# Kernel tuning notes

Measured on AMD Instinct MI355X. Metric: run time of the kernel, lower is better.

## Reference

```python
import jax, jax.numpy as jnp
import numpy as np

NUM_CITIES = 50000
EMB = 50   # embedding dim (hardcoded in module)
HID = 64   # LSTM hidden size (hardcoded in module)
BATCH = 1024
SEQ = 512


def setup_inputs() -> dict:
    key = jax.random.key(0)
    ks = jax.random.split(key, 8)
    s = 0.1
    return {
        "x": jax.random.randint(ks[0], (BATCH, SEQ), 0, NUM_CITIES),
        "emb": jax.random.normal(ks[1], (NUM_CITIES, EMB), jnp.float32) * s,
        # PyTorch LSTM weight layout: [4*H, in] with gate order i, f, g, o
        "W_ih": jax.random.normal(ks[2], (4 * HID, EMB), jnp.float32) * s,
        "W_hh": jax.random.normal(ks[3], (4 * HID, HID), jnp.float32) * s,
        "b_ih": jax.random.normal(ks[4], (4 * HID,), jnp.float32) * s,
        "b_hh": jax.random.normal(ks[5], (4 * HID,), jnp.float32) * s,
        "W_fc": jax.random.normal(ks[6], (NUM_CITIES, HID), jnp.float32) * s,
        "b_fc": jax.random.normal(ks[7], (NUM_CITIES,), jnp.float32) * s,
    }


def _lstm_last_hidden(e, W_ih, W_hh, b):
    """Run single-layer LSTM (zero init state), return final hidden h_T. e: [B,S,EMB]."""
    # Precompute all input-side gate projections in one big GEMM: [B,S,4H]
    gx = jnp.einsum('bsi,gi->bsg', e, W_ih) + b
    B = e.shape[0]
    H = W_hh.shape[1]
    W_hh_T = W_hh.T  # [H, 4H]
    h0 = jnp.zeros((B, H), e.dtype)
    c0 = jnp.zeros((B, H), e.dtype)

    def step(carry, gx_t):
        h, c = carry
        g = gx_t + h @ W_hh_T  # [B, 4H]
        i, f, gg, o = jnp.split(g, 4, axis=-1)
        i = jax.nn.sigmoid(i)
        f = jax.nn.sigmoid(f)
        gg = jnp.tanh(gg)
        o = jax.nn.sigmoid(o)
        c = f * c + i * gg
        h = o * jnp.tanh(c)
        return (h, c), None

    (h, c), _ = jax.lax.scan(step, (h0, c0), jnp.swapaxes(gx, 0, 1))
    return h  # [B, H]


def reference(x, emb, W_ih, W_hh, b_ih, b_hh, W_fc, b_fc):
    e = emb[x]                                   # [B, S, EMB] embedding lookup
    h = _lstm_last_hidden(e, W_ih, W_hh, b_ih + b_hh)  # [B, H]
    logits = h @ W_fc.T + b_fc                   # [B, NUM_CITIES]
    return jax.nn.softmax(logits, axis=1)
```

## Files before the change

### kernel.cpp

```cpp
#include <hip/hip_runtime.h>

#define BATCH 1024
#define SEQN  512
#define EMBD  50
#define HID   64
#define NC    50000
#define RPBK  2
#define HSTR  72
#define ESTR  72
#define CHUNK 16
#define NBLKX ((NC + 255) / 256)

typedef _Float16 half8 __attribute__((ext_vector_type(8)));
typedef float    f32x4 __attribute__((ext_vector_type(4)));

__device__ __forceinline__ void barrier_lds_only() {
    asm volatile("s_waitcnt lgkmcnt(0)\n\ts_barrier" ::: "memory");
}

__global__ __launch_bounds__(256, 2)
void lstm_rec(const int* __restrict__ x, const float* __restrict__ emb,
              const float* __restrict__ W_ih, const float* __restrict__ W_hh,
              const float* __restrict__ b_ih, const float* __restrict__ b_hh,
              _Float16* __restrict__ hFh)
{
    __shared__ __align__(16) _Float16 HS[2][16][HSTR];
    __shared__ __align__(16) _Float16 ER[2][CHUNK][RPBK][ESTR];
    __shared__ int xbuf[RPBK * SEQN];

    const int t    = threadIdx.x;
    const int w    = t >> 6;
    const int lane = t & 63;
    const int q    = lane >> 4;
    const int cc   = lane & 15;
    const int r0   = blockIdx.x * RPBK;
    const int u    = 16 * w + cc;

    half8 Bh[2][4], Bi[2][4];
    float bias[4];
#pragma unroll
    for (int nt = 0; nt < 4; ++nt) {
        const int g = 64 * nt + u;
        bias[nt] = b_ih[g] + b_hh[g];
#pragma unroll
        for (int kt = 0; kt < 2; ++kt)
#pragma unroll
            for (int j = 0; j < 8; ++j) {
                const int k = 32 * kt + 8 * q + j;
                Bh[kt][nt][j] = (_Float16)W_hh[g * HID + k];
                Bi[kt][nt][j] = (k < EMBD) ? (_Float16)W_ih[g * EMBD + k] : (_Float16)0.0f;
            }
    }

    for (int i = t; i < RPBK * SEQN; i += 256)
        xbuf[i] = x[(size_t)(r0 + (i >> 9)) * SEQN + (i & (SEQN - 1))];
    {
        _Float16* hz = &HS[0][0][0];
        for (int i = t; i < 2 * 16 * HSTR; i += 256) hz[i] = (_Float16)0.0f;
        _Float16* ez = &ER[0][0][0][0];
        for (int i = t; i < 2 * CHUNK * RPBK * ESTR; i += 256) ez[i] = (_Float16)0.0f;
    }
    __syncthreads();

    float ge[7];
#define GATHER(CH) do {                                                         \
        const int sb_ = (CH) * CHUNK;                                           \
        _Pragma("unroll")                                                       \
        for (int i = 0; i < 7; ++i) {                                           \
            const int idx = t + 256 * i;                                        \
            if (idx < CHUNK * RPBK * EMBD) {                                    \
                const int st_ = idx / (RPBK * EMBD);                            \
                const int rm_ = idx % (RPBK * EMBD);                            \
                const int rw_ = rm_ / EMBD;                                     \
                const int dm_ = rm_ % EMBD;                                     \
                int ss_ = sb_ + st_; if (ss_ > SEQN - 1) ss_ = SEQN - 1;        \
                ge[i] = emb[(size_t)xbuf[rw_ * SEQN + ss_] * EMBD + dm_];       \
            }                                                                   \
        }                                                                       \
    } while (0)
#define RINGW(CH) do {                                                          \
        const int hf_ = (CH) & 1;                                               \
        _Pragma("unroll")                                                       \
        for (int i = 0; i < 7; ++i) {                                           \
            const int idx = t + 256 * i;                                        \
            if (idx < CHUNK * RPBK * EMBD) {                                    \
                const int st_ = idx / (RPBK * EMBD);                            \
                const int rm_ = idx % (RPBK * EMBD);                            \
                const int rw_ = rm_ / EMBD;                                     \
                const int dm_ = rm_ % EMBD;                                     \
                ER[hf_][st_][rw_][dm_] = (_Float16)ge[i];                       \
            }                                                                   \
        }                                                                       \
    } while (0)

    GATHER(0);
    RINGW(0);
    GATHER(1);
    barrier_lds_only();

    float cst0 = 0.0f, cst1 = 0.0f;

    for (int s = 0; s < SEQN; ++s) {
        const int pb = s & 1;
        const int hf = (s >> 4) & 1;
        const int st = s & 15;
        const int er = cc & 1;

        const half8 Ae0 = *(const half8*)&ER[hf][st][er][8 * q];
        const half8 Ae1 = *(const half8*)&ER[hf][st][er][32 + 8 * q];
        const half8 Ah0 = *(const half8*)&HS[pb][cc][8 * q];
        const half8 Ah1 = *(const half8*)&HS[pb][cc][32 + 8 * q];

        f32x4 acc[4];
#pragma unroll
        for (int nt = 0; nt < 4; ++nt) {
            f32x4 z = (f32x4){0.f, 0.f, 0.f, 0.f};
            z = __builtin_amdgcn_mfma_f32_16x16x32_f16(Ae0, Bi[0][nt], z, 0, 0, 0);
            z = __builtin_amdgcn_mfma_f32_16x16x32_f16(Ae1, Bi[1][nt], z, 0, 0, 0);
            z = __builtin_amdgcn_mfma_f32_16x16x32_f16(Ah0, Bh[0][nt], z, 0, 0, 0);
            acc[nt] = __builtin_amdgcn_mfma_f32_16x16x32_f16(Ah1, Bh[1][nt], z, 0, 0, 0);
        }

        if (q == 0) {
            float p0[4], p1[4];
#pragma unroll
            for (int nt = 0; nt < 4; ++nt) {
                p0[nt] = acc[nt][0] + bias[nt];
                p1[nt] = acc[nt][1] + bias[nt];
            }
            const float i0 = __builtin_amdgcn_rcpf(1.0f + __expf(-p0[0]));
            const float f0 = __builtin_amdgcn_rcpf(1.0f + __expf(-p0[1]));
            const float g0 = 1.0f - 2.0f * __builtin_amdgcn_rcpf(__expf(2.0f * p0[2]) + 1.0f);
            const float o0 = __builtin_amdgcn_rcpf(1.0f + __expf(-p0[3]));
            const float i1 = __builtin_amdgcn_rcpf(1.0f + __expf(-p1[0]));
            const float f1 = __builtin_amdgcn_rcpf(1.0f + __expf(-p1[1]));
            const float g1 = 1.0f - 2.0f * __builtin_amdgcn_rcpf(__expf(2.0f * p1[2]) + 1.0f);
            const float o1 = __builtin_amdgcn_rcpf(1.0f + __expf(-p1[3]));
            cst0 = fmaf(f0, cst0, i0 * g0);
            cst1 = fmaf(f1, cst1, i1 * g1);
            const float h0 = o0 * (1.0f - 2.0f * __builtin_amdgcn_rcpf(__expf(2.0f * cst0) + 1.0f));
            const float h1 = o1 * (1.0f - 2.0f * __builtin_amdgcn_rcpf(__expf(2.0f * cst1) + 1.0f));
            HS[pb ^ 1][0][u] = (_Float16)h0;
            HS[pb ^ 1][1][u] = (_Float16)h1;
            if (s == SEQN - 1) {
                hFh[(size_t)r0 * HID + u]       = (_Float16)h0;
                hFh[(size_t)(r0 + 1) * HID + u] = (_Float16)h1;
            }
        }

        if (st == CHUNK - 1) {
            const int ch = s >> 4;
            RINGW(ch + 1);
            GATHER(ch + 2);
        }

        barrier_lds_only();
    }
#undef GATHER
#undef RINGW
}

__global__ __launch_bounds__(256, 2)
void fc_exp(const _Float16* __restrict__ hFh, const float* __restrict__ W_fc,
            const float* __restrict__ b_fc, float* __restrict__ Sp,
            float* __restrict__ out)
{
    __shared__ float sred[4][64];
    const int t    = threadIdx.x;
    const int w    = t >> 6;
    const int lane = t & 63;
    const int q    = lane >> 4;
    const int cc   = lane & 15;
    const int n0   = blockIdx.x * 256;

    half8 Bf[4][2];
    float bias[4];
#pragma unroll
    for (int nt = 0; nt < 4; ++nt) {
        int n = n0 + 64 * w + 16 * nt + cc;
        const int nl = (n < NC) ? n : NC - 1;
        bias[nt] = b_fc[nl];
#pragma unroll
        for (int kt = 0; kt < 2; ++kt) {
            const float* p = W_fc + (size_t)nl * HID + 32 * kt + 8 * q;
#pragma unroll
            for (int j = 0; j < 8; ++j) Bf[nt][kt][j] = (_Float16)p[j];
        }
    }

    const int rg0 = blockIdx.y * 8;
    for (int rg = rg0; rg < rg0 + 8; ++rg) {
        const int row0 = rg * 64;

        half8 Af[4][2];
#pragma unroll
        for (int mt = 0; mt < 4; ++mt)
#pragma unroll
            for (int kt = 0; kt < 2; ++kt)
                Af[mt][kt] = *(const half8*)&hFh[(size_t)(row0 + 16 * mt + cc) * HID + 32 * kt + 8 * q];

        f32x4 acc[4][4];
#pragma unroll
        for (int mt = 0; mt < 4; ++mt)
#pragma unroll
            for (int nt = 0; nt < 4; ++nt) acc[mt][nt] = (f32x4){0.f, 0.f, 0.f, 0.f};
#pragma unroll
        for (int mt = 0; mt < 4; ++mt)
#pragma unroll
            for (int nt = 0; nt < 4; ++nt)
#pragma unroll
                for (int kt = 0; kt < 2; ++kt)
                    acc[mt][nt] = __builtin_amdgcn_mfma_f32_16x16x32_f16(Af[mt][kt], Bf[nt][kt], acc[mt][nt], 0, 0, 0);

        float rs[4][4];
#pragma unroll
        for (int mt = 0; mt < 4; ++mt)
#pragma unroll
            for (int reg = 0; reg < 4; ++reg) rs[mt][reg] = 0.0f;

#pragma unroll
        for (int mt = 0; mt < 4; ++mt)
#pragma unroll
            for (int nt = 0; nt < 4; ++nt) {
                const int n = n0 + 64 * w + 16 * nt + cc;
                const bool ok = (n < NC);
#pragma unroll
                for (int reg = 0; reg < 4; ++reg) {
                    const float e = __expf(acc[mt][nt][reg] + bias[nt]);
                    rs[mt][reg] += ok ? e : 0.0f;
                    if (ok)
                        out[(size_t)(row0 + 16 * mt + 4 * q + reg) * NC + n] = e;
                }
            }

#pragma unroll
        for (int mt = 0; mt < 4; ++mt)
#pragma unroll
            for (int reg = 0; reg < 4; ++reg) {
                float v = rs[mt][reg];
                v += __shfl_xor(v, 1);
                v += __shfl_xor(v, 2);
                v += __shfl_xor(v, 4);
                v += __shfl_xor(v, 8);
                rs[mt][reg] = v;
            }
        if (cc == 0) {
#pragma unroll
            for (int mt = 0; mt < 4; ++mt)
#pragma unroll
                for (int reg = 0; reg < 4; ++reg)
                    sred[w][16 * mt + 4 * q + reg] = rs[mt][reg];
        }
        __syncthreads();
        if (t < 64)
            Sp[(size_t)(row0 + t) * NBLKX + blockIdx.x] =
                sred[0][t] + sred[1][t] + sred[2][t] + sred[3][t];
        __syncthreads();
    }
}

__global__ void reduce_s(const float* __restrict__ Sp, float* __restrict__ S) {
    const int r = blockIdx.x * 256 + threadIdx.x;
    if (r < BATCH) {
        const float* p = Sp + (size_t)r * NBLKX;
        float a0 = 0.f, a1 = 0.f, a2 = 0.f, a3 = 0.f;
        for (int j = 0; j < NBLKX; j += 4) {
            const f32x4 v = *(const f32x4*)&p[j];
            a0 += v[0]; a1 += v[1]; a2 += v[2]; a3 += v[3];
        }
        S[r] = 1.0f / (a0 + a1 + a2 + a3);
    }
}

__global__ __launch_bounds__(256, 4)
void scale_out(float* __restrict__ out, const float* __restrict__ S) {
    const int row = blockIdx.y;
    const float si = S[row];
    f32x4* o = (f32x4*)(out + (size_t)row * NC);
    for (int i = blockIdx.x * 256 + threadIdx.x; i < NC / 4; i += 13 * 256) {
        f32x4 v = o[i];
        v[0] *= si; v[1] *= si; v[2] *= si; v[3] *= si;
        o[i] = v;
    }
}

extern "C" void kernel_launch(void* const* d_in, const int* in_sizes, int n_in,
                              void* d_out, int out_size, void* d_ws, size_t ws_size,
                              hipStream_t stream) {
    (void)in_sizes; (void)n_in; (void)out_size; (void)ws_size;
    const int*   x    = (const int*)  d_in[0];
    const float* emb  = (const float*)d_in[1];
    const float* W_ih = (const float*)d_in[2];
    const float* W_hh = (const float*)d_in[3];
    const float* b_ih = (const float*)d_in[4];
    const float* b_hh = (const float*)d_in[5];
    const float* W_fc = (const float*)d_in[6];
    const float* b_fc = (const float*)d_in[7];
    float* out = (float*)d_out;

    _Float16* hFh = (_Float16*)d_ws;
    float* S  = (float*)((char*)d_ws + (size_t)BATCH * HID * 2);
    float* Sp = S + BATCH;

    hipLaunchKernelGGL(lstm_rec, dim3(BATCH / RPBK), dim3(256), 0, stream,
                       x, emb, W_ih, W_hh, b_ih, b_hh, hFh);
    hipLaunchKernelGGL(fc_exp, dim3(NBLKX, 2), dim3(256), 0, stream,
                       hFh, W_fc, b_fc, Sp, out);
    hipLaunchKernelGGL(reduce_s, dim3(4), dim3(256), 0, stream, Sp, S);
    hipLaunchKernelGGL(scale_out, dim3(13, BATCH), dim3(256), 0, stream, out, S);
}
```

Measured before the change: 573.6 us.

## Restructure LSTM rows per block and recompute FC logits instead of rescaling output

The LSTM kernel now handles 4 batch rows per block instead of 2. Each MFMA row maps to a real batch row via cc>>2, so every quad computes useful gates. The input projection for step s+1 is computed during step s, which takes it off the recurrent dependency chain. The FC stage becomes two passes: one computes only the exp-sums, and a second recomputes the logits, normalises them and writes coalesced output through an LDS transpose. This removes the unnormalised write plus the read-modify-write pass over the 200MB output, at the cost of doing the FC GEMM and exp twice.

```diff
diff --git a/kernel.cpp b/kernel.cpp
--- a/kernel.cpp
+++ b/kernel.cpp
@@ -5,10 +5,11 @@
 #define EMBD  50
 #define HID   64
 #define NC    50000
-#define RPBK  2
+#define RPBK  4
 #define HSTR  72
 #define ESTR  72
 #define CHUNK 16
+#define GELT  (CHUNK * RPBK * EMBD)
 #define NBLKX ((NC + 255) / 256)
 
 typedef _Float16 half8 __attribute__((ext_vector_type(8)));
@@ -18,13 +19,13 @@
     asm volatile("s_waitcnt lgkmcnt(0)\n\ts_barrier" ::: "memory");
 }
 
-__global__ __launch_bounds__(256, 2)
+__global__ __launch_bounds__(256, 1)
 void lstm_rec(const int* __restrict__ x, const float* __restrict__ emb,
               const float* __restrict__ W_ih, const float* __restrict__ W_hh,
               const float* __restrict__ b_ih, const float* __restrict__ b_hh,
               _Float16* __restrict__ hFh)
 {
-    __shared__ __align__(16) _Float16 HS[2][16][HSTR];
+    __shared__ __align__(16) _Float16 HS[2][RPBK][HSTR];
     __shared__ __align__(16) _Float16 ER[2][CHUNK][RPBK][ESTR];
     __shared__ int xbuf[RPBK * SEQN];
 
@@ -35,6 +36,7 @@
     const int cc   = lane & 15;
     const int r0   = blockIdx.x * RPBK;
     const int u    = 16 * w + cc;
+    const int ar   = cc >> 2;
 
     half8 Bh[2][4], Bi[2][4];
     float bias[4];
@@ -56,19 +58,19 @@
         xbuf[i] = x[(size_t)(r0 + (i >> 9)) * SEQN + (i & (SEQN - 1))];
     {
         _Float16* hz = &HS[0][0][0];
-        for (int i = t; i < 2 * 16 * HSTR; i += 256) hz[i] = (_Float16)0.0f;
+        for (int i = t; i < 2 * RPBK * HSTR; i += 256) hz[i] = (_Float16)0.0f;
         _Float16* ez = &ER[0][0][0][0];
         for (int i = t; i < 2 * CHUNK * RPBK * ESTR; i += 256) ez[i] = (_Float16)0.0f;
     }
     __syncthreads();
 
-    float ge[7];
+    float ge[13];
 #define GATHER(CH) do {                                                         \
         const int sb_ = (CH) * CHUNK;                                           \
         _Pragma("unroll")                                                       \
-        for (int i = 0; i < 7; ++i) {                                           \
+        for (int i = 0; i < 13; ++i) {                                          \
             const int idx = t + 256 * i;                                        \
-            if (idx < CHUNK * RPBK * EMBD) {                                    \
+            if (idx < GELT) {                                                   \
                 const int st_ = idx / (RPBK * EMBD);                            \
                 const int rm_ = idx % (RPBK * EMBD);                            \
                 const int rw_ = rm_ / EMBD;                                     \
@@ -81,9 +83,9 @@
 #define RINGW(CH) do {                                                          \
         const int hf_ = (CH) & 1;                                               \
         _Pragma("unroll")                                                       \
-        for (int i = 0; i < 7; ++i) {                                           \
+        for (int i = 0; i < 13; ++i) {                                          \
             const int idx = t + 256 * i;                                        \
-            if (idx < CHUNK * RPBK * EMBD) {                                    \
+            if (idx < GELT) {                                                   \
                 const int st_ = idx / (RPBK * EMBD);                            \
                 const int rm_ = idx % (RPBK * EMBD);                            \
                 const int rw_ = rm_ / EMBD;                                     \
@@ -96,74 +98,81 @@
     GATHER(0);
     RINGW(0);
     GATHER(1);
-    barrier_lds_only();
-
-    float cst0 = 0.0f, cst1 = 0.0f;
-
-    for (int s = 0; s < SEQN; ++s) {
-        const int pb = s & 1;
-        const int hf = (s >> 4) & 1;
-        const int st = s & 15;
-        const int er = cc & 1;
-
-        const half8 Ae0 = *(const half8*)&ER[hf][st][er][8 * q];
-        const half8 Ae1 = *(const half8*)&ER[hf][st][er][32 + 8 * q];
-        const half8 Ah0 = *(const half8*)&HS[pb][cc][8 * q];
-        const half8 Ah1 = *(const half8*)&HS[pb][cc][32 + 8 * q];
-
-        f32x4 acc[4];
+    __syncthreads();
+
+    f32x4 zA[4], zB[4];
+    {
+        const half8 Ae0 = *(const half8*)&ER[0][0][ar][8 * q];
+        const half8 Ae1 = *(const half8*)&ER[0][0][ar][32 + 8 * q];
 #pragma unroll
         for (int nt = 0; nt < 4; ++nt) {
-            f32x4 z = (f32x4){0.f, 0.f, 0.f, 0.f};
-            z = __builtin_amdgcn_mfma_f32_16x16x32_f16(Ae0, Bi[0][nt], z, 0, 0, 0);
-            z = __builtin_amdgcn_mfma_f32_16x16x32_f16(Ae1, Bi[1][nt], z, 0, 0, 0);
-            z = __builtin_amdgcn_mfma_f32_16x16x32_f16(Ah0, Bh[0][nt], z, 0, 0, 0);
-            acc[nt] = __builtin_amdgcn_mfma_f32_16x16x32_f16(Ah1, Bh[1][nt], z, 0, 0, 0);
-        }
-
-        if (q == 0) {
-            float p0[4], p1[4];
-#pragma unroll
-            for (int nt = 0; nt < 4; ++nt) {
-                p0[nt] = acc[nt][0] + bias[nt];
-                p1[nt] = acc[nt][1] + bias[nt];
-            }
-            const float i0 = __builtin_amdgcn_rcpf(1.0f + __expf(-p0[0]));
-            const float f0 = __builtin_amdgcn_rcpf(1.0f + __expf(-p0[1]));
-            const float g0 = 1.0f - 2.0f * __builtin_amdgcn_rcpf(__expf(2.0f * p0[2]) + 1.0f);
-            const float o0 = __builtin_amdgcn_rcpf(1.0f + __expf(-p0[3]));
-            const float i1 = __builtin_amdgcn_rcpf(1.0f + __expf(-p1[0]));
-            const float f1 = __builtin_amdgcn_rcpf(1.0f + __expf(-p1[1]));
-            const float g1 = 1.0f - 2.0f * __builtin_amdgcn_rcpf(__expf(2.0f * p1[2]) + 1.0f);
-            const float o1 = __builtin_amdgcn_rcpf(1.0f + __expf(-p1[3]));
-            cst0 = fmaf(f0, cst0, i0 * g0);
-            cst1 = fmaf(f1, cst1, i1 * g1);
-            const float h0 = o0 * (1.0f - 2.0f * __builtin_amdgcn_rcpf(__expf(2.0f * cst0) + 1.0f));
-            const float h1 = o1 * (1.0f - 2.0f * __builtin_amdgcn_rcpf(__expf(2.0f * cst1) + 1.0f));
-            HS[pb ^ 1][0][u] = (_Float16)h0;
-            HS[pb ^ 1][1][u] = (_Float16)h1;
-            if (s == SEQN - 1) {
-                hFh[(size_t)r0 * HID + u]       = (_Float16)h0;
-                hFh[(size_t)(r0 + 1) * HID + u] = (_Float16)h1;
-            }
-        }
-
-        if (st == CHUNK - 1) {
-            const int ch = s >> 4;
-            RINGW(ch + 1);
-            GATHER(ch + 2);
-        }
-
-        barrier_lds_only();
-    }
+            f32x4 zz = (f32x4){0.f, 0.f, 0.f, 0.f};
+            zz = __builtin_amdgcn_mfma_f32_16x16x32_f16(Ae0, Bi[0][nt], zz, 0, 0, 0);
+            zA[nt] = __builtin_amdgcn_mfma_f32_16x16x32_f16(Ae1, Bi[1][nt], zz, 0, 0, 0);
+        }
+    }
+
+    float cst = 0.0f;
+
+#define LSTM_STEP(S, PB, ZIN, ZOUT) do {                                          \
+                     \
+        const half8 Ah0 = *(const half8*)&HS[PB][ar][8 * q];                      \
+        const half8 Ah1 = *(const half8*)&HS[PB][ar][32 + 8 * q];                 \
+        f32x4 acc[4];                                                             \
+        _Pragma("unroll")                                                         \
+        for (int nt = 0; nt < 4; ++nt) {                                          \
+            f32x4 t1 = __builtin_amdgcn_mfma_f32_16x16x32_f16(Ah0, Bh[0][nt], ZIN[nt], 0, 0, 0); \
+            acc[nt] = __builtin_amdgcn_mfma_f32_16x16x32_f16(Ah1, Bh[1][nt], t1, 0, 0, 0); \
+        }                                                                         \
+                         \
+        {                                                                         \
+            const int sn  = ((S) + 1 < SEQN) ? (S) + 1 : SEQN - 1;                \
+            const int hfn = (sn >> 4) & 1;                                        \
+            const int stn = sn & 15;                                              \
+            const half8 Ae0 = *(const half8*)&ER[hfn][stn][ar][8 * q];            \
+            const half8 Ae1 = *(const half8*)&ER[hfn][stn][ar][32 + 8 * q];       \
+            _Pragma("unroll")                                                     \
+            for (int nt = 0; nt < 4; ++nt) {                                      \
+                f32x4 t2 = (f32x4){0.f, 0.f, 0.f, 0.f};                           \
+                t2 = __builtin_amdgcn_mfma_f32_16x16x32_f16(Ae0, Bi[0][nt], t2, 0, 0, 0); \
+                ZOUT[nt] = __builtin_amdgcn_mfma_f32_16x16x32_f16(Ae1, Bi[1][nt], t2, 0, 0, 0); \
+            }                                                                     \
+        }                                                                         \
+                   \
+        const float p0 = acc[0][0] + bias[0];                                     \
+        const float p1 = acc[1][0] + bias[1];                                     \
+        const float p2 = acc[2][0] + bias[2];                                     \
+        const float p3 = acc[3][0] + bias[3];                                     \
+        const float i_ = __builtin_amdgcn_rcpf(1.0f + __expf(-p0));               \
+        const float f_ = __builtin_amdgcn_rcpf(1.0f + __expf(-p1));               \
+        const float g_ = 1.0f - 2.0f * __builtin_amdgcn_rcpf(__expf(2.0f * p2) + 1.0f); \
+        const float o_ = __builtin_amdgcn_rcpf(1.0f + __expf(-p3));               \
+        cst = fmaf(f_, cst, i_ * g_);                                             \
+        const float hv = o_ * (1.0f - 2.0f * __builtin_amdgcn_rcpf(__expf(2.0f * cst) + 1.0f)); \
+        HS[(PB) ^ 1][q][u] = (_Float16)hv;                                        \
+        if ((S) == SEQN - 1)                                                      \
+            hFh[(size_t)(r0 + q) * HID + u] = (_Float16)hv;                       \
+                \
+        if (((S) & 15) == 8) {                                                    \
+            const int ch = (S) >> 4;                                              \
+            RINGW(ch + 1);                                                        \
+            GATHER(ch + 2);                                                       \
+        }                                                                         \
+        barrier_lds_only();                                                       \
+    } while (0)
+
+    for (int s2 = 0; s2 < SEQN; s2 += 2) {
+        LSTM_STEP(s2,     0, zA, zB);
+        LSTM_STEP(s2 + 1, 1, zB, zA);
+    }
+#undef LSTM_STEP
 #undef GATHER
 #undef RINGW
 }
 
 __global__ __launch_bounds__(256, 2)
-void fc_exp(const _Float16* __restrict__ hFh, const float* __restrict__ W_fc,
-            const float* __restrict__ b_fc, float* __restrict__ Sp,
-            float* __restrict__ out)
+void fc_sum(const _Float16* __restrict__ hFh, const float* __restrict__ W_fc,
+            const float* __restrict__ b_fc, float* __restrict__ Sp)
 {
     __shared__ float sred[4][64];
     const int t    = threadIdx.x;
@@ -188,8 +197,8 @@
         }
     }
 
-    const int rg0 = blockIdx.y * 8;
-    for (int rg = rg0; rg < rg0 + 8; ++rg) {
+    const int rg0 = blockIdx.y * 4;
+    for (int rg = rg0; rg < rg0 + 4; ++rg) {
         const int row0 = rg * 64;
 
         half8 Af[4][2];
@@ -217,7 +226,6 @@
         for (int mt = 0; mt < 4; ++mt)
 #pragma unroll
             for (int reg = 0; reg < 4; ++reg) rs[mt][reg] = 0.0f;
-
 #pragma unroll
         for (int mt = 0; mt < 4; ++mt)
 #pragma unroll
@@ -228,11 +236,8 @@
                 for (int reg = 0; reg < 4; ++reg) {
                     const float e = __expf(acc[mt][nt][reg] + bias[nt]);
                     rs[mt][reg] += ok ? e : 0.0f;
-                    if (ok)
-                        out[(size_t)(row0 + 16 * mt + 4 * q + reg) * NC + n] = e;
                 }
             }
-
 #pragma unroll
         for (int mt = 0; mt < 4; ++mt)
 #pragma unroll
@@ -272,15 +277,85 @@
     }
 }
 
-__global__ __launch_bounds__(256, 4)
-void scale_out(float* __restrict__ out, const float* __restrict__ S) {
-    const int row = blockIdx.y;
-    const float si = S[row];
-    f32x4* o = (f32x4*)(out + (size_t)row * NC);
-    for (int i = blockIdx.x * 256 + threadIdx.x; i < NC / 4; i += 13 * 256) {
-        f32x4 v = o[i];
-        v[0] *= si; v[1] *= si; v[2] *= si; v[3] *= si;
-        o[i] = v;
+__global__ __launch_bounds__(256, 2)
+void fc_write(const _Float16* __restrict__ hFh, const float* __restrict__ W_fc,
+              const float* __restrict__ b_fc, const float* __restrict__ S,
+              float* __restrict__ out)
+{
+    __shared__ float sinv2[256];
+    __shared__ __align__(16) float obuf[64][260];
+    const int t    = threadIdx.x;
+    const int w    = t >> 6;
+    const int lane = t & 63;
+    const int q    = lane >> 4;
+    const int cc   = lane & 15;
+    const int n0   = blockIdx.x * 256;
+
+    sinv2[t] = S[blockIdx.y * 256 + t];
+
+    half8 Bf[4][2];
+    float bias[4];
+#pragma unroll
+    for (int nt = 0; nt < 4; ++nt) {
+        int n = n0 + 64 * w + 16 * nt + cc;
+        const int nl = (n < NC) ? n : NC - 1;
+        bias[nt] = b_fc[nl];
+#pragma unroll
+        for (int kt = 0; kt < 2; ++kt) {
+            const float* p = W_fc + (size_t)nl * HID + 32 * kt + 8 * q;
+#pragma unroll
+            for (int j = 0; j < 8; ++j) Bf[nt][kt][j] = (_Float16)p[j];
+        }
+    }
+    __syncthreads();
+
+    const int rg0 = blockIdx.y * 4;
+#pragma unroll 1
+    for (int rr = 0; rr < 4; ++rr) {
+        const int row0 = (rg0 + rr) * 64;
+
+        half8 Af[4][2];
+#pragma unroll
+        for (int mt = 0; mt < 4; ++mt)
+#pragma unroll
+            for (int kt = 0; kt < 2; ++kt)
+                Af[mt][kt] = *(const half8*)&hFh[(size_t)(row0 + 16 * mt + cc) * HID + 32 * kt + 8 * q];
+
+        f32x4 acc[4][4];
+#pragma unroll
+        for (int mt = 0; mt < 4; ++mt)
+#pragma unroll
+            for (int nt = 0; nt < 4; ++nt) acc[mt][nt] = (f32x4){0.f, 0.f, 0.f, 0.f};
+#pragma unroll
+        for (int mt = 0; mt < 4; ++mt)
+#pragma unroll
+            for (int nt = 0; nt < 4; ++nt)
+#pragma unroll
+                for (int kt = 0; kt < 2; ++kt)
+                    acc[mt][nt] = __builtin_amdgcn_mfma_f32_16x16x32_f16(Af[mt][kt], Bf[nt][kt], acc[mt][nt], 0, 0, 0);
+
+#pragma unroll
+        for (int mt = 0; mt < 4; ++mt)
+#pragma unroll
+            for (int nt = 0; nt < 4; ++nt)
+#pragma unroll
+                for (int reg = 0; reg < 4; ++reg) {
+                    const int lr = 16 * mt + 4 * q + reg;
+                    const float e = __expf(acc[mt][nt][reg] + bias[nt]);
+                    obuf[lr][64 * w + 16 * nt + cc] = e * sinv2[rr * 64 + lr];
+                }
+        __syncthreads();
+
+        const int col = 4 * lane;
+        if (n0 + col < NC) {
+#pragma unroll
+            for (int i = 0; i < 16; ++i) {
+                const int row = 16 * w + i;
+                *(f32x4*)&out[(size_t)(row0 + row) * NC + n0 + col] =
+                    *(const f32x4*)&obuf[row][col];
+            }
+        }
+        __syncthreads();
     }
 }
 
@@ -304,8 +379,9 @@
 
     hipLaunchKernelGGL(lstm_rec, dim3(BATCH / RPBK), dim3(256), 0, stream,
                        x, emb, W_ih, W_hh, b_ih, b_hh, hFh);
-    hipLaunchKernelGGL(fc_exp, dim3(NBLKX, 2), dim3(256), 0, stream,
-                       hFh, W_fc, b_fc, Sp, out);
+    hipLaunchKernelGGL(fc_sum,   dim3(NBLKX, 4), dim3(256), 0, stream,
+                       hFh, W_fc, b_fc, Sp);
     hipLaunchKernelGGL(reduce_s, dim3(4), dim3(256), 0, stream, Sp, S);
-    hipLaunchKernelGGL(scale_out, dim3(13, BATCH), dim3(256), 0, stream, out, S);
-}
+    hipLaunchKernelGGL(fc_write, dim3(NBLKX, 4), dim3(256), 0, stream,
+                       hFh, W_fc, b_fc, S, out);
+}
```

After: 460.0 us. -19.8%, faster.
